# Performance work log

Measured on AMD Instinct MI355X. Metric: run time of the kernel, lower is better.

## Reference

```python
import jax, jax.numpy as jnp
import numpy as np

B, N = 64, 32768

def setup_inputs() -> dict:
    key = jax.random.key(0)
    k1, k2, k3, k4 = jax.random.split(key, 4)
    audio = jax.random.normal(k1, (B, N), dtype=jnp.float32)
    g = jax.random.uniform(k2, (B, N, 1), dtype=jnp.float32)
    twoR = jax.random.uniform(k3, (B, N, 1), dtype=jnp.float32)
    mix = jax.random.uniform(k4, (B, N, 3), dtype=jnp.float32)
    return {"audio": audio, "g": g, "twoR": twoR, "mix": mix}


def _svf(audio, g, twoR, mix):
    b, n = audio.shape
    T = 1.0 / (1.0 + g * (g + twoR))                      # [B,N,1]
    ones = jnp.ones_like(g)
    # H: [B,N,2,2] time-varying state matrix
    H = T[..., None] * jnp.concatenate(
        [ones, -g, g, twoR * g + 1.0], axis=-1).reshape(b, n, 2, 2)
    gHB = (g * T) * jnp.concatenate([ones, g], axis=-1)   # [B,N,2]
    gHBx = gHB * audio[..., None]                          # [B,N,2]

    # Linear time-varying recurrence: Y_t = gHBx_t + H_t @ s_{t-1}; s_t = 2 Y_t - s_{t-1}
    def step(state, inp):
        Ht, ut = inp                                       # [B,2,2], [B,2]
        Yt = ut + jnp.einsum('bij,bj->bi', Ht, state)
        return 2.0 * Yt - state, Yt

    s0 = jnp.ones((b, 2), dtype=audio.dtype)
    _, Y = jax.lax.scan(step,
                        s0,
                        (jnp.moveaxis(H, 1, 0), jnp.moveaxis(gHBx, 1, 0)))
    Y = jnp.moveaxis(Y, 0, 1)                              # [B,N,2]

    twoR_ = twoR[..., 0]                                   # [B,N]
    y_bp, y_lp = Y[..., 0], Y[..., 1]
    y_hp = audio - twoR_ * y_bp - y_lp
    y_mixed = twoR_ * mix[..., 0] * y_bp + mix[..., 1] * y_lp + mix[..., 2] * y_hp
    return y_mixed


def reference(audio, g, twoR, mix):
    return _svf(audio, g, twoR, mix)
```

## Files before the change

kernel.cpp:

```cpp
#include <hip/hip_runtime.h>


#define BATCH     64
#define SEQ       32768
#define CHUNKS    16
#define CHUNK_LEN (SEQ / CHUNKS)
#define TPB       256
#define STEPS     (CHUNK_LEN / TPB)
#define NBLK      (BATCH * CHUNKS)

struct Aff { float a00, a01, a10, a11, b0, b1; };

__device__ __forceinline__ Aff compose(const Aff l, const Aff e) {
    Aff r;
    r.a00 = fmaf(l.a00, e.a00, l.a01 * e.a10);
    r.a01 = fmaf(l.a00, e.a01, l.a01 * e.a11);
    r.a10 = fmaf(l.a10, e.a00, l.a11 * e.a10);
    r.a11 = fmaf(l.a10, e.a01, l.a11 * e.a11);
    r.b0  = fmaf(l.a00, e.b0, fmaf(l.a01, e.b1, l.b0));
    r.b1  = fmaf(l.a10, e.b0, fmaf(l.a11, e.b1, l.b1));
    return r;
}

__device__ __forceinline__ Aff step_affine(float gi, float Ri, float xi) {
    float T  = 1.0f / fmaf(gi, gi + Ri, 1.0f);
    float Tg = T * gi;
    Aff r;
    r.a00 = 2.0f * T - 1.0f;
    r.a01 = -2.0f * Tg;
    r.a10 = 2.0f * Tg;
    r.a11 = 2.0f * fmaf(Tg, Ri, T) - 1.0f;
    r.b0  = 2.0f * Tg * xi;
    r.b1  = gi * r.b0;
    return r;
}

__device__ __forceinline__ Aff block_scan_incl(Aff v, Aff (*buf)[TPB], int t) {
    int src = 0;
    buf[0][t] = v;
    __syncthreads();
#pragma unroll
    for (int off = 1; off < TPB; off <<= 1) {
        Aff cur = buf[src][t];
        int idx = (t >= off) ? (t - off) : 0;
        Aff prev = buf[src][idx];
        Aff res = (t >= off) ? compose(cur, prev) : cur;
        buf[1 - src][t] = res;
        src ^= 1;
        __syncthreads();
    }
    return buf[src][t];
}

__device__ __forceinline__ void load8(const float* __restrict__ p, int base, float v[8]) {
    float4 a = *reinterpret_cast<const float4*>(p + base);
    float4 b = *reinterpret_cast<const float4*>(p + base + 4);
    v[0]=a.x; v[1]=a.y; v[2]=a.z; v[3]=a.w; v[4]=b.x; v[5]=b.y; v[6]=b.z; v[7]=b.w;
}

__global__ __launch_bounds__(TPB) void svf_chunk_reduce(
    const float* __restrict__ audio, const float* __restrict__ g,
    const float* __restrict__ twoR, Aff* __restrict__ chunk_comp)
{
    __shared__ Aff buf[2][TPB];
    const int t    = threadIdx.x;
    const int base = blockIdx.x * CHUNK_LEN + t * STEPS;

    float gv[STEPS], rv[STEPS], xv[STEPS];
    load8(g, base, gv); load8(twoR, base, rv); load8(audio, base, xv);

    Aff acc = step_affine(gv[0], rv[0], xv[0]);
#pragma unroll
    for (int i = 1; i < STEPS; ++i)
        acc = compose(step_affine(gv[i], rv[i], xv[i]), acc);

    Aff tot = block_scan_incl(acc, buf, t);
    if (t == TPB - 1) chunk_comp[blockIdx.x] = tot;
}

__global__ __launch_bounds__(TPB) void svf_emit(
    const float* __restrict__ audio, const float* __restrict__ g,
    const float* __restrict__ twoR, const float* __restrict__ mix,
    const Aff* __restrict__ chunk_comp, float* __restrict__ out)
{
    __shared__ Aff buf[2][TPB];
    const int blk  = blockIdx.x;
    const int b    = blk / CHUNKS;
    const int t    = threadIdx.x;
    const int base = blk * CHUNK_LEN + t * STEPS;

    float gv[STEPS], rv[STEPS], xv[STEPS];
    load8(g, base, gv); load8(twoR, base, rv); load8(audio, base, xv);

    Aff acc = step_affine(gv[0], rv[0], xv[0]);
#pragma unroll
    for (int i = 1; i < STEPS; ++i)
        acc = compose(step_affine(gv[i], rv[i], xv[i]), acc);

    Aff incl = block_scan_incl(acc, buf, t);
    buf[0][t] = incl;
    __syncthreads();

    float cs0 = 1.0f, cs1 = 1.0f;
    for (int cc = b * CHUNKS; cc < blk; ++cc) {
        Aff a = chunk_comp[cc];
        float n0 = fmaf(a.a00, cs0, fmaf(a.a01, cs1, a.b0));
        float n1 = fmaf(a.a10, cs0, fmaf(a.a11, cs1, a.b1));
        cs0 = n0; cs1 = n1;
    }

    float s0, s1;
    if (t == 0) { s0 = cs0; s1 = cs1; }
    else {
        Aff p = buf[0][t - 1];
        s0 = fmaf(p.a00, cs0, fmaf(p.a01, cs1, p.b0));
        s1 = fmaf(p.a10, cs0, fmaf(p.a11, cs1, p.b1));
    }

    const float4* m4 = reinterpret_cast<const float4*>(mix + 3 * base);
    float mv[24];
#pragma unroll
    for (int q = 0; q < 6; ++q) {
        float4 m = m4[q];
        mv[4*q+0]=m.x; mv[4*q+1]=m.y; mv[4*q+2]=m.z; mv[4*q+3]=m.w;
    }

    float ov[STEPS];
#pragma unroll
    for (int i = 0; i < STEPS; ++i) {
        float gi = gv[i], Ri = rv[i], xi = xv[i];
        float T  = 1.0f / fmaf(gi, gi + Ri, 1.0f);
        float w  = fmaf(gi, xi, s0);
        float Y0 = T * fmaf(-gi, s1, w);
        float Y1 = T * fmaf(gi, w, fmaf(Ri, gi, 1.0f) * s1);
        float hp = xi - Ri * Y0 - Y1;
        ov[i] = fmaf(Ri * mv[3*i], Y0, fmaf(mv[3*i+1], Y1, mv[3*i+2] * hp));
        s0 = fmaf(2.0f, Y0, -s0);
        s1 = fmaf(2.0f, Y1, -s1);
    }

    *reinterpret_cast<float4*>(out + base)     = make_float4(ov[0], ov[1], ov[2], ov[3]);
    *reinterpret_cast<float4*>(out + base + 4) = make_float4(ov[4], ov[5], ov[6], ov[7]);
}

extern "C" void kernel_launch(void* const* d_in, const int* in_sizes, int n_in,
                              void* d_out, int out_size, void* d_ws, size_t ws_size,
                              hipStream_t stream) {
    const float* audio = (const float*)d_in[0];
    const float* g     = (const float*)d_in[1];
    const float* twoR  = (const float*)d_in[2];
    const float* mix   = (const float*)d_in[3];
    float* out = (float*)d_out;
    Aff* chunk_comp = (Aff*)d_ws;

    svf_chunk_reduce<<<NBLK, TPB, 0, stream>>>(audio, g, twoR, chunk_comp);
    svf_emit<<<NBLK, TPB, 0, stream>>>(audio, g, twoR, mix, chunk_comp, out);
}
```

Baseline: 96.40 us.

## Fuse reduce and emit kernels into single-pass scan with inter-block flag signaling

Merges the two-kernel chunked scan into one kernel where each block publishes its chunk aggregate to global memory with a release flag, and later chunks spin-wait on their predecessors' flags. This removes the second read of g, twoR and audio and one kernel launch, and the mix load is moved earlier to overlap with the scan. It adds a memset per call and depends on blocks being scheduled in order so the spin-waits do not deadlock; the serial lookback chain could also cost latency.

```diff
diff --git a/kernel.cpp b/kernel.cpp
--- a/kernel.cpp
+++ b/kernel.cpp
@@ -58,39 +58,29 @@
     v[0]=a.x; v[1]=a.y; v[2]=a.z; v[3]=a.w; v[4]=b.x; v[5]=b.y; v[6]=b.z; v[7]=b.w;
 }
 
-__global__ __launch_bounds__(TPB) void svf_chunk_reduce(
+__global__ __launch_bounds__(TPB, 4) void svf_fused(
     const float* __restrict__ audio, const float* __restrict__ g,
-    const float* __restrict__ twoR, Aff* __restrict__ chunk_comp)
+    const float* __restrict__ twoR, const float* __restrict__ mix,
+    float* __restrict__ agg, int* __restrict__ flags,
+    float* __restrict__ out)
 {
     __shared__ Aff buf[2][TPB];
-    const int t    = threadIdx.x;
-    const int base = blockIdx.x * CHUNK_LEN + t * STEPS;
-
-    float gv[STEPS], rv[STEPS], xv[STEPS];
-    load8(g, base, gv); load8(twoR, base, rv); load8(audio, base, xv);
-
-    Aff acc = step_affine(gv[0], rv[0], xv[0]);
-#pragma unroll
-    for (int i = 1; i < STEPS; ++i)
-        acc = compose(step_affine(gv[i], rv[i], xv[i]), acc);
-
-    Aff tot = block_scan_incl(acc, buf, t);
-    if (t == TPB - 1) chunk_comp[blockIdx.x] = tot;
-}
-
-__global__ __launch_bounds__(TPB) void svf_emit(
-    const float* __restrict__ audio, const float* __restrict__ g,
-    const float* __restrict__ twoR, const float* __restrict__ mix,
-    const Aff* __restrict__ chunk_comp, float* __restrict__ out)
-{
-    __shared__ Aff buf[2][TPB];
+    __shared__ Aff preds[CHUNKS];
     const int blk  = blockIdx.x;
-    const int b    = blk / CHUNKS;
+    const int c    = blk & (CHUNKS - 1);
     const int t    = threadIdx.x;
     const int base = blk * CHUNK_LEN + t * STEPS;
 
     float gv[STEPS], rv[STEPS], xv[STEPS];
     load8(g, base, gv); load8(twoR, base, rv); load8(audio, base, xv);
+
+    const float4* m4 = reinterpret_cast<const float4*>(mix + 3 * base);
+    float mv[24];
+#pragma unroll
+    for (int q = 0; q < 6; ++q) {
+        float4 m = m4[q];
+        mv[4*q+0]=m.x; mv[4*q+1]=m.y; mv[4*q+2]=m.z; mv[4*q+3]=m.w;
+    }
 
     Aff acc = step_affine(gv[0], rv[0], xv[0]);
 #pragma unroll
@@ -98,12 +88,33 @@
         acc = compose(step_affine(gv[i], rv[i], xv[i]), acc);
 
     Aff incl = block_scan_incl(acc, buf, t);
+
+    if (t == TPB - 1 && c != CHUNKS - 1) {
+        float* dst = agg + 6 * blk;
+        const float* s = (const float*)&incl;
+#pragma unroll
+        for (int k = 0; k < 6; ++k)
+            __hip_atomic_store(dst + k, s[k], __ATOMIC_RELAXED, __HIP_MEMORY_SCOPE_AGENT);
+        __hip_atomic_store(&flags[blk], 1, __ATOMIC_RELEASE, __HIP_MEMORY_SCOPE_AGENT);
+    }
+
     buf[0][t] = incl;
+
+    if (t < c) {
+        const int p = blk - c + t;
+        while (__hip_atomic_load(&flags[p], __ATOMIC_ACQUIRE, __HIP_MEMORY_SCOPE_AGENT) == 0)
+            __builtin_amdgcn_s_sleep(8);
+        const float* s = agg + 6 * p;
+        float* d = (float*)&preds[t];
+#pragma unroll
+        for (int k = 0; k < 6; ++k)
+            d[k] = __hip_atomic_load(s + k, __ATOMIC_RELAXED, __HIP_MEMORY_SCOPE_AGENT);
+    }
     __syncthreads();
 
     float cs0 = 1.0f, cs1 = 1.0f;
-    for (int cc = b * CHUNKS; cc < blk; ++cc) {
-        Aff a = chunk_comp[cc];
+    for (int j = 0; j < c; ++j) {
+        Aff a = preds[j];
         float n0 = fmaf(a.a00, cs0, fmaf(a.a01, cs1, a.b0));
         float n1 = fmaf(a.a10, cs0, fmaf(a.a11, cs1, a.b1));
         cs0 = n0; cs1 = n1;
@@ -115,14 +126,6 @@
         Aff p = buf[0][t - 1];
         s0 = fmaf(p.a00, cs0, fmaf(p.a01, cs1, p.b0));
         s1 = fmaf(p.a10, cs0, fmaf(p.a11, cs1, p.b1));
-    }
-
-    const float4* m4 = reinterpret_cast<const float4*>(mix + 3 * base);
-    float mv[24];
-#pragma unroll
-    for (int q = 0; q < 6; ++q) {
-        float4 m = m4[q];
-        mv[4*q+0]=m.x; mv[4*q+1]=m.y; mv[4*q+2]=m.z; mv[4*q+3]=m.w;
     }
 
     float ov[STEPS];
@@ -151,8 +154,10 @@
     const float* twoR  = (const float*)d_in[2];
     const float* mix   = (const float*)d_in[3];
     float* out = (float*)d_out;
-    Aff* chunk_comp = (Aff*)d_ws;
 
-    svf_chunk_reduce<<<NBLK, TPB, 0, stream>>>(audio, g, twoR, chunk_comp);
-    svf_emit<<<NBLK, TPB, 0, stream>>>(audio, g, twoR, mix, chunk_comp, out);
+    float* agg  = (float*)d_ws;
+    int*   flags = (int*)((char*)d_ws + NBLK * sizeof(Aff));
+
+    hipMemsetAsync(flags, 0, NBLK * sizeof(int), stream);
+    svf_fused<<<NBLK, TPB, 0, stream>>>(audio, g, twoR, mix, agg, flags, out);
 }
```

After: 134.3 us. 1.39x slower.

## Use wavefront shuffle scans and double chunk count for SVF scan

Applied to the files above, without the earlier changes.

Replaces the shared-memory Hillis-Steele block scan, which needs a barrier per step, with 64-lane shuffle scans plus a small cross-wave combine in shared memory. The chunk count doubles, so each thread handles 4 samples and twice as many blocks run. The serial per-block loop over earlier chunk aggregates becomes a parallel wave scan. This cuts LDS traffic and barriers and raises parallelism, in exchange for more redundant affine composition and shuffle work.

```diff
diff --git a/kernel.cpp b/kernel.cpp
--- a/kernel.cpp
+++ b/kernel.cpp
@@ -3,13 +3,19 @@
 
 #define BATCH     64
 #define SEQ       32768
-#define CHUNKS    16
+#define CHUNKS    32
 #define CHUNK_LEN (SEQ / CHUNKS)
 #define TPB       256
+#define NWAVE     (TPB / 64)
 #define STEPS     (CHUNK_LEN / TPB)
 #define NBLK      (BATCH * CHUNKS)
 
 struct Aff { float a00, a01, a10, a11, b0, b1; };
+
+__device__ __forceinline__ Aff aff_ident() {
+    Aff r; r.a00 = 1.f; r.a01 = 0.f; r.a10 = 0.f; r.a11 = 1.f; r.b0 = 0.f; r.b1 = 0.f;
+    return r;
+}
 
 __device__ __forceinline__ Aff compose(const Aff l, const Aff e) {
     Aff r;
@@ -35,95 +41,117 @@
     return r;
 }
 
-__device__ __forceinline__ Aff block_scan_incl(Aff v, Aff (*buf)[TPB], int t) {
-    int src = 0;
-    buf[0][t] = v;
-    __syncthreads();
-#pragma unroll
-    for (int off = 1; off < TPB; off <<= 1) {
-        Aff cur = buf[src][t];
-        int idx = (t >= off) ? (t - off) : 0;
-        Aff prev = buf[src][idx];
-        Aff res = (t >= off) ? compose(cur, prev) : cur;
-        buf[1 - src][t] = res;
-        src ^= 1;
-        __syncthreads();
-    }
-    return buf[src][t];
+__device__ __forceinline__ Aff shfl_up_aff(const Aff v, int d) {
+    Aff r;
+    r.a00 = __shfl_up(v.a00, d); r.a01 = __shfl_up(v.a01, d);
+    r.a10 = __shfl_up(v.a10, d); r.a11 = __shfl_up(v.a11, d);
+    r.b0  = __shfl_up(v.b0,  d); r.b1  = __shfl_up(v.b1,  d);
+    return r;
 }
 
-__device__ __forceinline__ void load8(const float* __restrict__ p, int base, float v[8]) {
-    float4 a = *reinterpret_cast<const float4*>(p + base);
-    float4 b = *reinterpret_cast<const float4*>(p + base + 4);
-    v[0]=a.x; v[1]=a.y; v[2]=a.z; v[3]=a.w; v[4]=b.x; v[5]=b.y; v[6]=b.z; v[7]=b.w;
+__device__ __forceinline__ Aff wave_scan_incl(Aff v, int lane) {
+#pragma unroll
+    for (int off = 1; off < 64; off <<= 1) {
+        Aff p = shfl_up_aff(v, off);
+        if (lane >= off) v = compose(v, p);
+    }
+    return v;
 }
 
-__global__ __launch_bounds__(TPB) void svf_chunk_reduce(
-    const float* __restrict__ audio, const float* __restrict__ g,
-    const float* __restrict__ twoR, Aff* __restrict__ chunk_comp)
-{
-    __shared__ Aff buf[2][TPB];
-    const int t    = threadIdx.x;
-    const int base = blockIdx.x * CHUNK_LEN + t * STEPS;
-
-    float gv[STEPS], rv[STEPS], xv[STEPS];
-    load8(g, base, gv); load8(twoR, base, rv); load8(audio, base, xv);
-
-    Aff acc = step_affine(gv[0], rv[0], xv[0]);
+__device__ __forceinline__ Aff local_affine(const float gv[4], const float rv[4],
+                                            const float xv[4]) {
+    Aff a = step_affine(gv[0], rv[0], xv[0]);
 #pragma unroll
     for (int i = 1; i < STEPS; ++i)
-        acc = compose(step_affine(gv[i], rv[i], xv[i]), acc);
-
-    Aff tot = block_scan_incl(acc, buf, t);
-    if (t == TPB - 1) chunk_comp[blockIdx.x] = tot;
+        a = compose(step_affine(gv[i], rv[i], xv[i]), a);
+    return a;
 }
 
-__global__ __launch_bounds__(TPB) void svf_emit(
+__global__ __launch_bounds__(TPB, 4) void svf_k1(
+    const float* __restrict__ audio, const float* __restrict__ g,
+    const float* __restrict__ twoR, float* __restrict__ agg)
+{
+    __shared__ Aff wtot[NWAVE];
+    const int blk  = blockIdx.x;
+    const int t    = threadIdx.x;
+    const int lane = t & 63, wave = t >> 6;
+    const int base = blk * CHUNK_LEN + t * STEPS;
+
+    float4 g4 = *reinterpret_cast<const float4*>(g + base);
+    float4 r4 = *reinterpret_cast<const float4*>(twoR + base);
+    float4 x4 = *reinterpret_cast<const float4*>(audio + base);
+    float gv[4] = {g4.x, g4.y, g4.z, g4.w};
+    float rv[4] = {r4.x, r4.y, r4.z, r4.w};
+    float xv[4] = {x4.x, x4.y, x4.z, x4.w};
+
+    Aff W = wave_scan_incl(local_affine(gv, rv, xv), lane);
+    if (lane == 63) wtot[wave] = W;
+    __syncthreads();
+
+    if (t == TPB - 1) {
+        Aff A = wtot[0];
+#pragma unroll
+        for (int w = 1; w < NWAVE; ++w) A = compose(wtot[w], A);
+        float* dst = agg + 6 * blk;
+        dst[0] = A.a00; dst[1] = A.a01; dst[2] = A.a10;
+        dst[3] = A.a11; dst[4] = A.b0;  dst[5] = A.b1;
+    }
+}
+
+__global__ __launch_bounds__(TPB, 4) void svf_k2(
     const float* __restrict__ audio, const float* __restrict__ g,
     const float* __restrict__ twoR, const float* __restrict__ mix,
-    const Aff* __restrict__ chunk_comp, float* __restrict__ out)
+    const float* __restrict__ agg, float* __restrict__ out)
 {
-    __shared__ Aff buf[2][TPB];
+    __shared__ Aff wtot[NWAVE];
+    __shared__ float csb[2];
     const int blk  = blockIdx.x;
-    const int b    = blk / CHUNKS;
+    const int c    = blk & (CHUNKS - 1);
     const int t    = threadIdx.x;
+    const int lane = t & 63, wave = t >> 6;
     const int base = blk * CHUNK_LEN + t * STEPS;
 
-    float gv[STEPS], rv[STEPS], xv[STEPS];
-    load8(g, base, gv); load8(twoR, base, rv); load8(audio, base, xv);
+    float4 g4 = *reinterpret_cast<const float4*>(g + base);
+    float4 r4 = *reinterpret_cast<const float4*>(twoR + base);
+    float4 x4 = *reinterpret_cast<const float4*>(audio + base);
+    float gv[4] = {g4.x, g4.y, g4.z, g4.w};
+    float rv[4] = {r4.x, r4.y, r4.z, r4.w};
+    float xv[4] = {x4.x, x4.y, x4.z, x4.w};
 
-    Aff acc = step_affine(gv[0], rv[0], xv[0]);
-#pragma unroll
-    for (int i = 1; i < STEPS; ++i)
-        acc = compose(step_affine(gv[i], rv[i], xv[i]), acc);
+    const float4* m4 = reinterpret_cast<const float4*>(mix + 3 * base);
+    float4 m0 = m4[0], m1 = m4[1], m2 = m4[2];
+    float mv[12] = {m0.x, m0.y, m0.z, m0.w, m1.x, m1.y,
+                    m1.z, m1.w, m2.x, m2.y, m2.z, m2.w};
 
-    Aff incl = block_scan_incl(acc, buf, t);
-    buf[0][t] = incl;
+    Aff W = wave_scan_incl(local_affine(gv, rv, xv), lane);
+    if (lane == 63) wtot[wave] = W;
+
+    if (wave == 0) {
+        Aff p = aff_ident();
+        if (lane < c) {
+            const float* s = agg + 6 * (blk - c + lane);
+            p.a00 = s[0]; p.a01 = s[1]; p.a10 = s[2];
+            p.a11 = s[3]; p.b0  = s[4]; p.b1  = s[5];
+        }
+        p = wave_scan_incl(p, lane);
+        const int src = (c > 0) ? (c - 1) : 0;
+        if (lane == src) {
+            csb[0] = p.a00 + p.a01 + p.b0;
+            csb[1] = p.a10 + p.a11 + p.b1;
+        }
+    }
     __syncthreads();
 
-    float cs0 = 1.0f, cs1 = 1.0f;
-    for (int cc = b * CHUNKS; cc < blk; ++cc) {
-        Aff a = chunk_comp[cc];
-        float n0 = fmaf(a.a00, cs0, fmaf(a.a01, cs1, a.b0));
-        float n1 = fmaf(a.a10, cs0, fmaf(a.a11, cs1, a.b1));
-        cs0 = n0; cs1 = n1;
-    }
+    const float cs0 = csb[0], cs1 = csb[1];
 
-    float s0, s1;
-    if (t == 0) { s0 = cs0; s1 = cs1; }
-    else {
-        Aff p = buf[0][t - 1];
-        s0 = fmaf(p.a00, cs0, fmaf(p.a01, cs1, p.b0));
-        s1 = fmaf(p.a10, cs0, fmaf(p.a11, cs1, p.b1));
-    }
+    Aff P = aff_ident();
+    for (int wj = 0; wj < wave; ++wj) P = compose(wtot[wj], P);
 
-    const float4* m4 = reinterpret_cast<const float4*>(mix + 3 * base);
-    float mv[24];
-#pragma unroll
-    for (int q = 0; q < 6; ++q) {
-        float4 m = m4[q];
-        mv[4*q+0]=m.x; mv[4*q+1]=m.y; mv[4*q+2]=m.z; mv[4*q+3]=m.w;
-    }
+    Aff Wp = shfl_up_aff(W, 1);
+    Aff E = (lane == 0) ? P : compose(Wp, P);
+
+    float s0 = fmaf(E.a00, cs0, fmaf(E.a01, cs1, E.b0));
+    float s1 = fmaf(E.a10, cs0, fmaf(E.a11, cs1, E.b1));
 
     float ov[STEPS];
 #pragma unroll
@@ -139,8 +167,7 @@
         s1 = fmaf(2.0f, Y1, -s1);
     }
 
-    *reinterpret_cast<float4*>(out + base)     = make_float4(ov[0], ov[1], ov[2], ov[3]);
-    *reinterpret_cast<float4*>(out + base + 4) = make_float4(ov[4], ov[5], ov[6], ov[7]);
+    *reinterpret_cast<float4*>(out + base) = make_float4(ov[0], ov[1], ov[2], ov[3]);
 }
 
 extern "C" void kernel_launch(void* const* d_in, const int* in_sizes, int n_in,
@@ -151,8 +178,8 @@
     const float* twoR  = (const float*)d_in[2];
     const float* mix   = (const float*)d_in[3];
     float* out = (float*)d_out;
-    Aff* chunk_comp = (Aff*)d_ws;
+    float* agg = (float*)d_ws;
 
-    svf_chunk_reduce<<<NBLK, TPB, 0, stream>>>(audio, g, twoR, chunk_comp);
-    svf_emit<<<NBLK, TPB, 0, stream>>>(audio, g, twoR, mix, chunk_comp, out);
+    svf_k1<<<NBLK, TPB, 0, stream>>>(audio, g, twoR, agg);
+    svf_k2<<<NBLK, TPB, 0, stream>>>(audio, g, twoR, mix, agg, out);
 }
```

New measurement: 97.19 us. Within noise of the previous version (+0.8%).
